# Kernel optimization log

Measured on AMD Instinct MI355X. Metric: run time of the kernel, lower is better.

The kernel has to match this reference:

```python
import jax, jax.numpy as jnp
import numpy as np

DIM = 2048
HEADS = 16
HD = DIM // HEADS
B = 1
S = 2560
L_CAP = 256
NAG_SCALE = 5.0
NAG_ALPHA = 0.25
NAG_TAU = 2.5
EPS_RMS = 1e-5


def setup_inputs() -> dict:
    key = jax.random.key(0)
    ks = jax.random.split(key, 6)
    h = jax.random.normal(ks[0], (B, S, DIM), dtype=jnp.float32)
    wq = jax.random.normal(ks[1], (DIM, DIM), dtype=jnp.float32) * 0.02
    wk = jax.random.normal(ks[2], (DIM, DIM), dtype=jnp.float32) * 0.02
    wv = jax.random.normal(ks[3], (DIM, DIM), dtype=jnp.float32) * 0.02
    wo = jax.random.normal(ks[4], (DIM, DIM), dtype=jnp.float32) * 0.02
    norm_q_w = jnp.ones((HD,), dtype=jnp.float32)
    norm_k_w = jnp.ones((HD,), dtype=jnp.float32)
    # real rotary angles: freqs_cis[b, s, d, 0]=cos, [...,1]=sin
    pos = jnp.arange(S, dtype=jnp.float32)[:, None]          # [S,1]
    inv_freq = 1.0 / (10000.0 ** (jnp.arange(HD // 2, dtype=jnp.float32) / (HD // 2)))
    ang = pos * inv_freq                                      # [S, HD/2]
    freqs_cis = jnp.stack([jnp.cos(ang), jnp.sin(ang)], axis=-1)[None]  # [1,S,HD/2,2]
    return {"h": h, "wq": wq, "wk": wk, "wv": wv, "wo": wo,
            "norm_q_w": norm_q_w, "norm_k_w": norm_k_w,
            "freqs_cis": freqs_cis, "cap_embed_len": L_CAP}


def _rmsnorm(x, w):
    # over last (head) dim
    return x * jax.lax.rsqrt(jnp.mean(x * x, axis=-1, keepdims=True) + EPS_RMS) * w


def _rope(x, freqs_cis):
    # x: [B,S,H,D]; freqs_cis: [1,S,D/2,2]
    xr = x.reshape(*x.shape[:-1], -1, 2)      # [B,S,H,D/2,2]
    cos = freqs_cis[..., 0][:, :, None, :]    # [1,S,1,D/2]
    sin = freqs_cis[..., 1][:, :, None, :]
    x0, x1 = xr[..., 0], xr[..., 1]
    o0 = x0 * cos - x1 * sin
    o1 = x1 * cos + x0 * sin
    return jnp.stack([o0, o1], axis=-1).reshape(x.shape)


def _sdpa(q, k, v):
    # q,k,v: [B,N,H,D] -> [B,N,H*D]
    scale = 1.0 / jnp.sqrt(jnp.asarray(q.shape[-1], q.dtype))
    s = jnp.einsum('bnhd,bmhd->bhnm', q, k) * scale
    a = jax.nn.softmax(s, axis=-1)
    o = jnp.einsum('bhnm,bmhd->bnhd', a, v)
    return o.reshape(o.shape[0], o.shape[1], -1)


def reference(h, wq, wk, wv, wo, norm_q_w, norm_k_w, freqs_cis, cap_embed_len):
    b, s, dim = h.shape
    q = (h @ wq.T).reshape(b, s, HEADS, HD)
    k = (h @ wk.T).reshape(b, s, HEADS, HD)
    v = (h @ wv.T).reshape(b, s, HEADS, HD)
    q = _rmsnorm(q, norm_q_w)
    k = _rmsnorm(k, norm_k_w)
    q = _rope(q, freqs_cis)
    k = _rope(k, freqs_cis)

    L = cap_embed_len
    # positive pass: drop trailing negative-caption tokens
    x_pos = _sdpa(q[:, :-L], k[:, :-L], v[:, :-L])            # [B,S-L,DIM]
    # swap positive caption slot for the negative caption
    q2 = q.at[:, -2 * L:-L].set(q[:, -L:])
    k2 = k.at[:, -2 * L:-L].set(k[:, -L:])
    v2 = v.at[:, -2 * L:-L].set(v[:, -L:])
    x_neg = _sdpa(q2[:, :-L], k2[:, :-L], v2[:, :-L])         # [B,S-L,DIM]
    x_neg_tail = x_neg[:, -L:]

    x_g = x_neg * (1.0 - NAG_SCALE) + x_pos * NAG_SCALE
    norm_pos = jnp.sum(jnp.abs(x_pos), axis=-1, keepdims=True)
    norm_g = jnp.sum(jnp.abs(x_g), axis=-1, keepdims=True)
    ratio = jnp.nan_to_num(norm_g / norm_pos, nan=10.0)
    factor = (1.0 / (norm_g + 1e-7)) * norm_pos * NAG_TAU
    x_g = jnp.where(ratio > NAG_TAU, x_g * factor, x_g)
    x_g = x_g * NAG_ALPHA + x_pos * (1.0 - NAG_ALPHA)

    out = jnp.concatenate([x_g, x_neg_tail], axis=1)          # [B,S,DIM]
    return out @ wo.T
```

## Files before the change

### kernel.cpp

```cpp
#include <hip/hip_runtime.h>
#include <stdint.h>


typedef short s8x __attribute__((ext_vector_type(8)));
typedef float f4x __attribute__((ext_vector_type(4)));
typedef unsigned short u16;

#define NDIM   2048
#define NHEAD  16
#define NHD    128
#define NSEQ   2560
#define NSDPA  2304

__device__ __forceinline__ u16 f2bf(float f) {
  union { float f; unsigned u; } v; v.f = f;
  unsigned r = v.u + 0x7FFFu + ((v.u >> 16) & 1u);
  return (u16)(r >> 16);
}

__device__ __forceinline__ void gload16(const void* g, void* l) {
  __builtin_amdgcn_global_load_lds(
      (const __attribute__((address_space(1))) unsigned*)g,
      (__attribute__((address_space(3))) unsigned*)l, 16, 0, 0);
}

__global__ void k_cvt(const float* __restrict__ src, u16* __restrict__ dst, int n8) {
  int i = blockIdx.x * blockDim.x + threadIdx.x;
  if (i >= n8) return;
  const float4* s4 = (const float4*)src + (size_t)i * 2;
  float4 a = s4[0], b = s4[1];
  uint4 p;
  p.x = (unsigned)f2bf(a.x) | ((unsigned)f2bf(a.y) << 16);
  p.y = (unsigned)f2bf(a.z) | ((unsigned)f2bf(a.w) << 16);
  p.z = (unsigned)f2bf(b.x) | ((unsigned)f2bf(b.y) << 16);
  p.w = (unsigned)f2bf(b.z) | ((unsigned)f2bf(b.w) << 16);
  *(uint4*)(dst + (size_t)i * 8) = p;
}

__global__ void k_cvt4(const float* __restrict__ w0, const float* __restrict__ w1,
                       const float* __restrict__ w2, const float* __restrict__ w3,
                       u16* __restrict__ dst) {
  int i = blockIdx.x * blockDim.x + threadIdx.x;
  int m = blockIdx.y;
  const float* src = (m == 0) ? w0 : (m == 1) ? w1 : (m == 2) ? w2 : w3;
  const float4* s4 = (const float4*)src + (size_t)i * 2;
  float4 a = s4[0], b = s4[1];
  uint4 p;
  p.x = (unsigned)f2bf(a.x) | ((unsigned)f2bf(a.y) << 16);
  p.y = (unsigned)f2bf(a.z) | ((unsigned)f2bf(a.w) << 16);
  p.z = (unsigned)f2bf(b.x) | ((unsigned)f2bf(b.y) << 16);
  p.w = (unsigned)f2bf(b.z) | ((unsigned)f2bf(b.w) << 16);
  *(uint4*)(dst + (size_t)m * 4194304 + (size_t)i * 8) = p;
}

__global__ __launch_bounds__(256, 2)
void k_gemm_bt(const u16* __restrict__ A, const u16* __restrict__ B,
               float* __restrict__ C, int K, int ldc) {
  __shared__ __align__(16) unsigned char sm[16384];
  const int bm = blockIdx.x * 128, bn = blockIdx.y * 128;
  const int lane = threadIdx.x & 63, wl = threadIdx.x >> 6;
  const int wm = wl >> 1, wn = wl & 1;
  const int g = lane >> 4, li = lane & 15;
  f4x acc[4][4] = {};
  const int nk = K >> 5;
  for (int kk = 0; kk < nk; ++kk) {
#pragma unroll
    for (int c = 0; c < 2; ++c) {
      int base = (wl * 2 + c) * 1024;
      int row = (base >> 6) + (lane >> 2);
      int colb = (lane & 3) * 16;
      gload16((const char*)A + ((size_t)(bm + row) * K + kk * 32) * 2 + colb, sm + base);
      gload16((const char*)B + ((size_t)(bn + row) * K + kk * 32) * 2 + colb, sm + 8192 + base);
    }
    __syncthreads();
    s8x a[4];
#pragma unroll
    for (int mt = 0; mt < 4; ++mt)
      a[mt] = *(const s8x*)(sm + (wm * 64 + mt * 16 + li) * 64 + g * 16);
#pragma unroll
    for (int nt = 0; nt < 4; ++nt) {
      s8x b = *(const s8x*)(sm + 8192 + (wn * 64 + nt * 16 + li) * 64 + g * 16);
#pragma unroll
      for (int mt = 0; mt < 4; ++mt)
        acc[mt][nt] = __builtin_amdgcn_mfma_f32_16x16x32_bf16(a[mt], b, acc[mt][nt], 0, 0, 0);
    }
    __syncthreads();
  }
#pragma unroll
  for (int mt = 0; mt < 4; ++mt)
#pragma unroll
    for (int nt = 0; nt < 4; ++nt)
#pragma unroll
      for (int r = 0; r < 4; ++r) {
        int row = bm + wm * 64 + mt * 16 + g * 4 + r;
        int col = bn + wn * 64 + nt * 16 + li;
        C[(size_t)row * ldc + col] = acc[mt][nt][r];
      }
}

__global__ void k_rmsrope(const float* __restrict__ qkv, const float* __restrict__ nqw,
                          const float* __restrict__ nkw, const float* __restrict__ fc,
                          u16* __restrict__ qh, u16* __restrict__ kh) {
  int wid = threadIdx.x >> 6, lane = threadIdx.x & 63;
  int pair = blockIdx.x * 4 + wid;
  int s = pair >> 4, hh = pair & 15;
  const float* qrow = qkv + (size_t)s * 6144 + hh * 128;
  float2 qv = *(const float2*)(qrow + lane * 2);
  float2 kv = *(const float2*)(qrow + 2048 + lane * 2);
  float sq = qv.x * qv.x + qv.y * qv.y;
  float sk = kv.x * kv.x + kv.y * kv.y;
#pragma unroll
  for (int m = 32; m >= 1; m >>= 1) { sq += __shfl_xor(sq, m); sk += __shfl_xor(sk, m); }
  float rq = rsqrtf(sq * (1.f / 128.f) + 1e-5f);
  float rk = rsqrtf(sk * (1.f / 128.f) + 1e-5f);
  float2 wq2 = *(const float2*)(nqw + lane * 2);
  float2 wk2 = *(const float2*)(nkw + lane * 2);
  float2 cs = *(const float2*)(fc + (size_t)s * 128 + lane * 2);
  float q0 = qv.x * rq * wq2.x, q1 = qv.y * rq * wq2.y;
  float k0 = kv.x * rk * wk2.x, k1 = kv.y * rk * wk2.y;
  unsigned qo = (unsigned)f2bf(q0 * cs.x - q1 * cs.y) | ((unsigned)f2bf(q1 * cs.x + q0 * cs.y) << 16);
  unsigned ko = (unsigned)f2bf(k0 * cs.x - k1 * cs.y) | ((unsigned)f2bf(k1 * cs.x + k0 * cs.y) << 16);
  *(unsigned*)(qh + ((size_t)hh * NSEQ + s) * 128 + lane * 2) = qo;
  *(unsigned*)(kh + ((size_t)hh * NSEQ + s) * 128 + lane * 2) = ko;
}

__global__ void k_vtrans(const float* __restrict__ qkv, u16* __restrict__ vT) {
  __shared__ u16 t[128][65];
  int s0 = blockIdx.x * 64, hh = blockIdx.y;
  int tid = threadIdx.x;
#pragma unroll
  for (int rep = 0; rep < 32; ++rep) {
    int idx = rep * 256 + tid; int sr = idx >> 7, d = idx & 127;
    t[d][sr] = f2bf(qkv[(size_t)(s0 + sr) * 6144 + 4096 + hh * 128 + d]);
  }
  __syncthreads();
#pragma unroll
  for (int rep = 0; rep < 16; ++rep) {
    int idx = rep * 256 + tid; int d = idx >> 5, sc2 = (idx & 31) * 2;
    unsigned val = (unsigned)t[d][sc2] | ((unsigned)t[d][sc2 + 1] << 16);
    *(unsigned*)(vT + ((size_t)hh * 128 + d) * NSEQ + s0 + sc2) = val;
  }
}

__device__ __forceinline__ void stage_kv(const u16* __restrict__ khh,
                                         const u16* __restrict__ vTh,
                                         int kphys, unsigned char* sm,
                                         int lane, int wl) {
#pragma unroll
  for (int c = 0; c < 4; ++c) {
    int base = (wl * 4 + c) * 1024;
    { int row = (base >> 8) + (lane >> 4);
      int src = ((lane & 15) * 16) ^ ((row & 7) << 4);
      gload16((const char*)(khh + (size_t)(kphys + row) * 128) + src, sm + base); }
    { int row = (base >> 7) + (lane >> 3);
      int src = ((lane & 7) * 16) ^ ((row & 7) << 4);
      gload16((const char*)(vTh + (size_t)row * NSEQ + kphys) + src, sm + 16384 + base); }
  }
}

__device__ __forceinline__ void tile_compute(unsigned char* sm, unsigned char* pb,
                                             const s8x (&aq)[4], int g, int li,
                                             f4x (&o)[9], float (&mold)[4]) {
  const float S2 = 0.08838834764831845f * 1.4426950408889634f;
  const float THR_RAW = 90.0f;
  const s8x PONE = {16256, 16256, 16256, 16256, 16256, 16256, 16256, 16256};
  const f4x zf = {0.f, 0.f, 0.f, 0.f};
  f4x sc[4];
#pragma unroll
  for (int nt = 0; nt < 4; ++nt) sc[nt] = zf;
  __builtin_amdgcn_s_setprio(1);
#pragma unroll
  for (int nt = 0; nt < 4; ++nt) {
    int row = nt * 16 + li;
    int rx = (row & 7) << 4;
#pragma unroll
    for (int ds = 0; ds < 4; ++ds) {
      s8x bk = *(const s8x*)(sm + row * 256 + ((ds * 64 + g * 16) ^ rx));
      sc[nt] = __builtin_amdgcn_mfma_f32_16x16x32_bf16(aq[ds], bk, sc[nt], 0, 0, 0);
    }
  }
  __builtin_amdgcn_s_setprio(0);

  float tl[4];
#pragma unroll
  for (int r = 0; r < 4; ++r)
    tl[r] = fmaxf(fmaxf(sc[0][r], sc[1][r]), fmaxf(sc[2][r], sc[3][r]));
  bool need = (tl[0] > mold[0] + THR_RAW) || (tl[1] > mold[1] + THR_RAW) ||
              (tl[2] > mold[2] + THR_RAW) || (tl[3] > mold[3] + THR_RAW);
  if (__any((int)need)) {
#pragma unroll
    for (int r = 0; r < 4; ++r) {
      float t = tl[r];
#pragma unroll
      for (int msk = 8; msk >= 1; msk >>= 1) t = fmaxf(t, __shfl_xor(t, msk));
      float mn = fmaxf(mold[r], t);
      float corr = exp2f((mold[r] - mn) * S2);
      mold[r] = mn;
#pragma unroll
      for (int dt = 0; dt < 9; ++dt) o[dt][r] *= corr;
    }
  }
  float nb[4];
#pragma unroll
  for (int r = 0; r < 4; ++r) nb[r] = -mold[r] * S2;
#pragma unroll
  for (int nt = 0; nt < 4; ++nt) {
    int colb = (nt * 16 + li) * 2;
#pragma unroll
    for (int r = 0; r < 4; ++r) {
      float p = exp2f(fmaf(sc[nt][r], S2, nb[r]));
      int q = g * 4 + r;
      *(u16*)(pb + q * 128 + (colb ^ ((q & 7) << 4))) = f2bf(p);
    }
  }
  __builtin_amdgcn_s_setprio(1);
#pragma unroll
  for (int ks = 0; ks < 2; ++ks) {
    s8x pa = *(const s8x*)(pb + li * 128 + ((ks * 64 + g * 16) ^ ((li & 7) << 4)));
#pragma unroll
    for (int dt = 0; dt < 8; ++dt) {
      int row = dt * 16 + li;
      s8x bv = *(const s8x*)(sm + 16384 + row * 128 + ((ks * 64 + g * 16) ^ ((row & 7) << 4)));
      o[dt] = __builtin_amdgcn_mfma_f32_16x16x32_bf16(pa, bv, o[dt], 0, 0, 0);
    }
    o[8] = __builtin_amdgcn_mfma_f32_16x16x32_bf16(pa, PONE, o[8], 0, 0, 0);
  }
  __builtin_amdgcn_s_setprio(0);
}

__device__ __forceinline__ void epilogue(float* __restrict__ out, int q0, int hh,
                                         int g, int li, const f4x (&o)[9]) {
  float inv[4];
#pragma unroll
  for (int r = 0; r < 4; ++r) inv[r] = 1.f / o[8][r];
#pragma unroll
  for (int dt = 0; dt < 8; ++dt)
#pragma unroll
    for (int r = 0; r < 4; ++r) {
      int n = q0 + g * 4 + r;
      int col = hh * 128 + dt * 16 + li;
      out[(size_t)n * NDIM + col] = o[dt][r] * inv[r];
    }
}

__global__ __launch_bounds__(256, 3)
void k_attn(const u16* __restrict__ qh, const u16* __restrict__ kh,
            const u16* __restrict__ vT, float* __restrict__ xpos,
            float* __restrict__ xneg) {
  __shared__ __align__(16) unsigned char sm[40960];
  const int lane = threadIdx.x & 63, wl = threadIdx.x >> 6;
  const int g = lane >> 4, li = lane & 15;

  const int s = blockIdx.x;
  const int xcd = s & 7, j = s >> 3;
  const int hh = 2 * xcd + (j & 1);
  const int u = j >> 1;
  const bool shared_blk = (u < 32);
  const int qb = shared_blk ? u : (32 + ((u - 32) >> 1));
  const int mode = shared_blk ? 0 : ((u - 32) & 1);
  const int q0 = qb * 64 + wl * 16;

  const u16* khh = kh + (size_t)hh * NSEQ * 128;
  const u16* vTh = vT + (size_t)hh * 128 * NSEQ;
  unsigned char* pb = sm + 32768 + wl * 2048;

  s8x aq[4];
  {
    int ql = q0 + li;
    int qp = (mode && ql >= 2048) ? ql + 256 : ql;
    const u16* base = qh + ((size_t)hh * NSEQ + qp) * 128 + g * 8;
#pragma unroll
    for (int ds = 0; ds < 4; ++ds) aq[ds] = *(const s8x*)(base + ds * 32);
  }

  const f4x zf = {0.f, 0.f, 0.f, 0.f};
  f4x o1[9];
  float m1[4];
#pragma unroll
  for (int dt = 0; dt < 9; ++dt) o1[dt] = zf;
#pragma unroll
  for (int r = 0; r < 4; ++r) m1[r] = -1e30f;

  const int n1 = shared_blk ? 32 : 36;
  for (int t = 0; t < n1; ++t) {
    int kphys = (mode && t >= 32) ? 2304 + (t - 32) * 64 : t * 64;
    stage_kv(khh, vTh, kphys, sm, lane, wl);
    __syncthreads();
    tile_compute(sm, pb, aq, g, li, o1, m1);
    __syncthreads();
  }

  if (shared_blk) {
    f4x o2[9];
    float m2[4];
#pragma unroll
    for (int dt = 0; dt < 9; ++dt) o2[dt] = o1[dt];
#pragma unroll
    for (int r = 0; r < 4; ++r) m2[r] = m1[r];
    for (int t = 0; t < 4; ++t) {
      stage_kv(khh, vTh, 2048 + t * 64, sm, lane, wl);
      __syncthreads();
      tile_compute(sm, pb, aq, g, li, o1, m1);
      __syncthreads();
    }
    epilogue(xpos, q0, hh, g, li, o1);
    for (int t = 0; t < 4; ++t) {
      stage_kv(khh, vTh, 2304 + t * 64, sm, lane, wl);
      __syncthreads();
      tile_compute(sm, pb, aq, g, li, o2, m2);
      __syncthreads();
    }
    epilogue(xneg, q0, hh, g, li, o2);
  } else {
    epilogue(mode ? xneg : xpos, q0, hh, g, li, o1);
  }
}

__global__ void k_nag(const float* __restrict__ xp, const float* __restrict__ xn,
                      u16* __restrict__ X) {
  int n = blockIdx.x, t = threadIdx.x;
  if (n >= NSDPA) {
    const float* src = xn + (size_t)(n - 256) * NDIM + t * 8;
    float4 a = *(const float4*)src, b = *(const float4*)(src + 4);
    uint4 p;
    p.x = (unsigned)f2bf(a.x) | ((unsigned)f2bf(a.y) << 16);
    p.y = (unsigned)f2bf(a.z) | ((unsigned)f2bf(a.w) << 16);
    p.z = (unsigned)f2bf(b.x) | ((unsigned)f2bf(b.y) << 16);
    p.w = (unsigned)f2bf(b.z) | ((unsigned)f2bf(b.w) << 16);
    *(uint4*)(X + (size_t)n * NDIM + t * 8) = p;
    return;
  }
  const float* pr = xp + (size_t)n * NDIM + t * 8;
  const float* nr = xn + (size_t)n * NDIM + t * 8;
  float4 a = *(const float4*)pr, b = *(const float4*)(pr + 4);
  float4 c = *(const float4*)nr, d = *(const float4*)(nr + 4);
  float pv[8] = {a.x, a.y, a.z, a.w, b.x, b.y, b.z, b.w};
  float nv[8] = {c.x, c.y, c.z, c.w, d.x, d.y, d.z, d.w};
  float gv[8];
  float sp = 0.f, sg = 0.f;
#pragma unroll
  for (int i = 0; i < 8; ++i) {
    float gq = 5.f * pv[i] - 4.f * nv[i];
    gv[i] = gq; sp += fabsf(pv[i]); sg += fabsf(gq);
  }
#pragma unroll
  for (int m = 32; m >= 1; m >>= 1) { sp += __shfl_xor(sp, m); sg += __shfl_xor(sg, m); }
  __shared__ float red[2][4];
  int wid = t >> 6, lane = t & 63;
  if (lane == 0) { red[0][wid] = sp; red[1][wid] = sg; }
  __syncthreads();
  float np_ = red[0][0] + red[0][1] + red[0][2] + red[0][3];
  float ng_ = red[1][0] + red[1][1] + red[1][2] + red[1][3];
  float ratio = ng_ / np_;
  if (isnan(ratio)) ratio = 10.f;
  float factor = np_ * 2.5f / (ng_ + 1e-7f);
  float mul = (ratio > 2.5f) ? factor : 1.f;
  uint4 p;
  u16 ob[8];
#pragma unroll
  for (int i = 0; i < 8; ++i) ob[i] = f2bf(gv[i] * mul * 0.25f + pv[i] * 0.75f);
  p.x = (unsigned)ob[0] | ((unsigned)ob[1] << 16);
  p.y = (unsigned)ob[2] | ((unsigned)ob[3] << 16);
  p.z = (unsigned)ob[4] | ((unsigned)ob[5] << 16);
  p.w = (unsigned)ob[6] | ((unsigned)ob[7] << 16);
  *(uint4*)(X + (size_t)n * NDIM + t * 8) = p;
}

extern "C" void kernel_launch(void* const* d_in, const int* in_sizes, int n_in,
                              void* d_out, int out_size, void* d_ws, size_t ws_size,
                              hipStream_t stream) {
  const float* h   = (const float*)d_in[0];
  const float* wq  = (const float*)d_in[1];
  const float* wk  = (const float*)d_in[2];
  const float* wv  = (const float*)d_in[3];
  const float* wo  = (const float*)d_in[4];
  const float* nqw = (const float*)d_in[5];
  const float* nkw = (const float*)d_in[6];
  const float* fc  = (const float*)d_in[7];
  (void)in_sizes; (void)n_in; (void)out_size; (void)ws_size;

  char* ws = (char*)d_ws;
  u16*   wB   = (u16*)ws;
  u16*   hB   = (u16*)(ws + 33554432);
  float* qkv  = (float*)(ws + 44040192);
  u16*   qh   = (u16*)(ws + 106954752);
  u16*   kh   = qh + (size_t)16 * 2560 * 128;
  u16*   vT   = kh + (size_t)16 * 2560 * 128;
  float* xpos = qkv;
  float* xneg = xpos + (size_t)NSDPA * NDIM;
  u16*   X    = hB;

  k_cvt<<<2560, 256, 0, stream>>>(h, hB, 655360);
  k_cvt4<<<dim3(2048, 4), 256, 0, stream>>>(wq, wk, wv, wo, wB);

  k_gemm_bt<<<dim3(20, 48), 256, 0, stream>>>(hB, wB, qkv, 2048, 6144);
  k_rmsrope<<<10240, 256, 0, stream>>>(qkv, nqw, nkw, fc, qh, kh);
  k_vtrans<<<dim3(40, 16), 256, 0, stream>>>(qkv, vT);
  k_attn<<<640, 256, 0, stream>>>(qh, kh, vT, xpos, xneg);
  k_nag<<<2560, 256, 0, stream>>>(xpos, xneg, X);
  k_gemm_bt<<<dim3(20, 16), 256, 0, stream>>>(X, wB + 12582912, (float*)d_out, 2048, 2048);
}
```

Measured before the change: 281.8 us.

## Use a double-buffered 256x256-tile GEMM kernel for the QKV projection

After: 271.5 us. 1.04x faster.

```diff
diff --git a/kernel.cpp b/kernel.cpp
--- a/kernel.cpp
+++ b/kernel.cpp
@@ -98,6 +98,133 @@
       }
 }
 
+__device__ __forceinline__ void stageAB256(const u16* __restrict__ M, int K,
+                                           int row0, int kk, unsigned char* dst,
+                                           int tid) {
+#pragma unroll
+  for (int c = 0; c < 4; ++c) {
+    int idx = c * 512 + tid;
+    int r = idx >> 3, cc = idx & 7;
+    gload16(M + (size_t)(row0 + r) * K + kk + ((cc ^ (r & 7)) * 8), dst + idx * 16);
+  }
+}
+
+#define G256_SYNC() do { __builtin_amdgcn_s_barrier();                        \
+    asm volatile("s_waitcnt lgkmcnt(0)" ::: "memory");                        \
+    __builtin_amdgcn_sched_barrier(0); } while (0)
+
+__global__ __launch_bounds__(512, 2)
+void k_gemm256(const u16* __restrict__ A, const u16* __restrict__ B,
+               float* __restrict__ C, int K, int ldc, int nbn) {
+  extern __shared__ __align__(16) unsigned char sm[];
+  const int tid = threadIdx.x;
+  const int lane = tid & 63, wid = tid >> 6;
+  const int g = lane >> 4, li = lane & 15;
+  const int wr = wid >> 2, wc = wid & 3;
+
+  const int cpx = gridDim.x >> 3;
+  const int f = blockIdx.x;
+  const int swz = (f & 7) * cpx + (f >> 3);
+  const int bm = (swz / nbn) * 256, bn = (swz % nbn) * 256;
+
+  f4x acc[8][4] = {};
+  const int nk = K >> 6;
+
+  stageAB256(A, K, bm, 0, sm, tid);
+  stageAB256(B, K, bn, 0, sm + 32768, tid);
+  stageAB256(A, K, bm, 64, sm + 65536, tid);
+  stageAB256(B, K, bn, 64, sm + 98304, tid);
+  asm volatile("s_waitcnt vmcnt(8)" ::: "memory");
+  __builtin_amdgcn_s_barrier();
+
+  for (int t = 0; t < nk; ++t) {
+    unsigned char* sA = sm + (t & 1) * 65536;
+    unsigned char* sB = sA + 32768;
+    s8x a[8][2], b[4][2];
+
+#pragma unroll
+    for (int mt = 0; mt < 4; ++mt) {
+      int r = wr * 128 + mt * 16 + li;
+#pragma unroll
+      for (int ks = 0; ks < 2; ++ks)
+        a[mt][ks] = *(const s8x*)(sA + r * 128 + (((ks * 4 + g) ^ (r & 7)) * 16));
+    }
+#pragma unroll
+    for (int nt = 0; nt < 4; ++nt) {
+      int r = wc * 64 + nt * 16 + li;
+      b[nt][0] = *(const s8x*)(sB + r * 128 + ((g ^ (r & 7)) * 16));
+    }
+    G256_SYNC();
+    __builtin_amdgcn_s_setprio(1);
+#pragma unroll
+    for (int nt = 0; nt < 4; ++nt)
+#pragma unroll
+      for (int mt = 0; mt < 4; ++mt)
+        acc[mt][nt] = __builtin_amdgcn_mfma_f32_16x16x32_bf16(a[mt][0], b[nt][0], acc[mt][nt], 0, 0, 0);
+    __builtin_amdgcn_s_setprio(0);
+    __builtin_amdgcn_s_barrier();
+
+#pragma unroll
+    for (int mt = 4; mt < 8; ++mt) {
+      int r = wr * 128 + mt * 16 + li;
+#pragma unroll
+      for (int ks = 0; ks < 2; ++ks)
+        a[mt][ks] = *(const s8x*)(sA + r * 128 + (((ks * 4 + g) ^ (r & 7)) * 16));
+    }
+#pragma unroll
+    for (int nt = 0; nt < 4; ++nt) {
+      int r = wc * 64 + nt * 16 + li;
+      b[nt][1] = *(const s8x*)(sB + r * 128 + (((4 + g) ^ (r & 7)) * 16));
+    }
+    G256_SYNC();
+    __builtin_amdgcn_s_setprio(1);
+#pragma unroll
+    for (int nt = 0; nt < 4; ++nt)
+#pragma unroll
+      for (int mt = 4; mt < 8; ++mt)
+        acc[mt][nt] = __builtin_amdgcn_mfma_f32_16x16x32_bf16(a[mt][0], b[nt][0], acc[mt][nt], 0, 0, 0);
+    __builtin_amdgcn_s_setprio(0);
+    __builtin_amdgcn_s_barrier();
+
+    if (t + 2 < nk) stageAB256(A, K, bm, (t + 2) * 64, sA, tid);
+    G256_SYNC();
+    __builtin_amdgcn_s_setprio(1);
+#pragma unroll
+    for (int nt = 0; nt < 4; ++nt)
+#pragma unroll
+      for (int mt = 0; mt < 4; ++mt)
+        acc[mt][nt] = __builtin_amdgcn_mfma_f32_16x16x32_bf16(a[mt][1], b[nt][1], acc[mt][nt], 0, 0, 0);
+    __builtin_amdgcn_s_setprio(0);
+    __builtin_amdgcn_s_barrier();
+
+    if (t + 2 < nk) stageAB256(B, K, bn, (t + 2) * 64, sB, tid);
+    G256_SYNC();
+    __builtin_amdgcn_s_setprio(1);
+#pragma unroll
+    for (int nt = 0; nt < 4; ++nt)
+#pragma unroll
+      for (int mt = 4; mt < 8; ++mt)
+        acc[mt][nt] = __builtin_amdgcn_mfma_f32_16x16x32_bf16(a[mt][1], b[nt][1], acc[mt][nt], 0, 0, 0);
+    __builtin_amdgcn_s_setprio(0);
+    if (t + 1 < nk) {
+      if (t + 2 < nk) asm volatile("s_waitcnt vmcnt(8)" ::: "memory");
+      else            asm volatile("s_waitcnt vmcnt(0)" ::: "memory");
+      __builtin_amdgcn_s_barrier();
+    }
+  }
+
+#pragma unroll
+  for (int mt = 0; mt < 8; ++mt)
+#pragma unroll
+    for (int nt = 0; nt < 4; ++nt)
+#pragma unroll
+      for (int rr = 0; rr < 4; ++rr) {
+        int row = bm + wr * 128 + mt * 16 + g * 4 + rr;
+        int col = bn + wc * 64 + nt * 16 + li;
+        C[(size_t)row * ldc + col] = acc[mt][nt][rr];
+      }
+}
+
 __global__ void k_rmsrope(const float* __restrict__ qkv, const float* __restrict__ nqw,
                           const float* __restrict__ nkw, const float* __restrict__ fc,
                           u16* __restrict__ qh, u16* __restrict__ kh) {
@@ -390,10 +517,17 @@
   float* xneg = xpos + (size_t)NSDPA * NDIM;
   u16*   X    = hB;
 
+  static bool attr_done = false;
+  if (!attr_done) {
+    hipFuncSetAttribute((const void*)k_gemm256,
+                        hipFuncAttributeMaxDynamicSharedMemorySize, 131072);
+    attr_done = true;
+  }
+
   k_cvt<<<2560, 256, 0, stream>>>(h, hB, 655360);
   k_cvt4<<<dim3(2048, 4), 256, 0, stream>>>(wq, wk, wv, wo, wB);
 
-  k_gemm_bt<<<dim3(20, 48), 256, 0, stream>>>(hB, wB, qkv, 2048, 6144);
+  k_gemm256<<<240, 512, 131072, stream>>>(hB, wB, qkv, 2048, 6144, 24);
   k_rmsrope<<<10240, 256, 0, stream>>>(qkv, nqw, nkw, fc, qh, kh);
   k_vtrans<<<dim3(40, 16), 256, 0, stream>>>(qkv, vT);
   k_attn<<<640, 256, 0, stream>>>(qh, kh, vT, xpos, xneg);
```
